# Kernel optimization log

Measured on AMD Instinct MI355X. Metric: run time of the kernel, lower is better.

Reference implementation:

```python
import jax, jax.numpy as jnp
import numpy as np

V = np.array([[1.0, 1.0, 1.0], [1.0, -1.0, 1.0], [1.0, 1.0, -1.0]], dtype=np.float32)


def _lin_combs(kernels: np.ndarray) -> np.ndarray:
    """Project (O, C, 3, 3) kernels onto inverse of the 9x9 GCK +/-1 basis.
    Returns (O, C*9) with layout c*9 + (3*i + j), matching the torch module."""
    O, C = kernels.shape[0], kernels.shape[1]
    # basis_flat[k=3i+j, p=3r+s] = V[i,r] * V[j,s]
    basis_flat = np.einsum('ir,js->ijrs', V, V).reshape(9, 9)
    basis_inv = np.linalg.inv(basis_flat)
    kflat = kernels.reshape(O, C, 9)
    comb = np.einsum('kp,ocp->ock', basis_inv, kflat)  # (O, C, 9)
    return np.ascontiguousarray(comb.reshape(O, C * 9))


def setup_inputs() -> dict:
    key = jax.random.key(0)
    k1, k2 = jax.random.split(key)
    B, C, O, H, W = 1, 64, 64, 514, 514
    x = jax.random.normal(k1, (B, C, H, W), dtype=jnp.float32)
    kernels = np.asarray(jax.random.normal(k2, (O, C, 3, 3), dtype=jnp.float32))
    linCombs = jnp.asarray(_lin_combs(kernels))  # (O, C*9)
    return {"input": x, "linCombs": linCombs}


def reference(input, linCombs):
    # GCK 3x3 conv: rowwise +/-1 stage -> colwise +/-1 stage -> linComb matmul.
    x = input
    B, C, H, W = x.shape
    O = linCombs.shape[0]
    Ho, Wo = H - 2, W - 2  # padding = 0
    Vj = jnp.asarray(V)
    # rowwise stage: convolve (cross-correlate) along rows with each +/-1 vector
    rows = jnp.stack([x[:, :, r:r + Ho, :] for r in range(3)])       # (3,B,C,Ho,W)
    rowwise = jnp.einsum('ir,rbchw->bcihw', Vj, rows)                 # (B,C,3,Ho,W)
    # colwise stage: convolve along columns with each +/-1 vector
    cols = jnp.stack([rowwise[..., s:s + Wo] for s in range(3)])      # (3,B,C,3,Ho,Wo)
    colwise = jnp.einsum('js,sbcihw->bcijhw', Vj, cols)               # (B,C,3,3,Ho,Wo)
    feats = colwise.reshape(B, C * 9, Ho * Wo)                        # k = c*9 + 3i + j
    out = jnp.einsum('ok,bkp->bop', linCombs, feats)
    return out.reshape(B, O, Ho, Wo)
```

## Files before the change

### kernel.cpp

```cpp
#include <hip/hip_runtime.h>
#include <hip/hip_bf16.h>


constexpr int kC = 64, kO = 64;
constexpr int kH = 514, kW = 514;
constexpr int kHO = 512, kWO = 512;
constexpr int kNPIX = kH * kW;

typedef __attribute__((ext_vector_type(8))) short short8;
typedef __attribute__((ext_vector_type(4))) float floatx4;

__device__ inline unsigned short f2bf(float f) {
    unsigned int u = __float_as_uint(f);
    unsigned int r = (u + 0x7fffu + ((u >> 16) & 1u)) >> 16;
    return (unsigned short)r;
}

__global__ void gck_wprep(const float* __restrict__ lin, unsigned short* __restrict__ w2) {
    int t = blockIdx.x * 256 + threadIdx.x;
    if (t >= kO * kC * 9) return;
    int tap = t % 9;
    int c   = (t / 9) % kC;
    int o   = t / (9 * kC);
    int r = tap / 3, s = tap % 3;
    const float Vm[3][3] = {{1.f, 1.f, 1.f}, {1.f, -1.f, 1.f}, {1.f, 1.f, -1.f}};
    float acc = 0.f;
#pragma unroll
    for (int i = 0; i < 3; i++)
#pragma unroll
        for (int j = 0; j < 3; j++)
            acc += lin[o * (kC * 9) + c * 9 + 3 * i + j] * Vm[i][r] * Vm[j][s];
    int kglob = tap * 64 + c;
    int ks = kglob >> 5, kg = (kglob >> 3) & 3, e = kglob & 7;
    w2[((ks * 4 + kg) * 64 + o) * 8 + e] = f2bf(acc);
}

__global__ __launch_bounds__(256, 3) void gck_conv(const float* __restrict__ x,
                                                   const unsigned short* __restrict__ w2,
                                                   float* __restrict__ out) {
    __shared__ unsigned short xs[6 * 66 * 64];

    const int bid = blockIdx.x;
    const int ct = bid & 7;
    const int rt = bid >> 3;
    const int hbase = rt * 4;
    const int wbase = ct * 64;
    const int t    = threadIdx.x;
    const int wave = t >> 6;
    const int lane = t & 63;
    const int l16  = lane & 15;
    const int kg   = lane >> 4;

    {
        const int w0 = lane;
#pragma unroll
        for (int p = 0; p < 24; ++p) {
            int idx = p * 4 + wave;
            int r   = idx >> 4;
            int cg  = idx & 15;
            int ch0 = cg * 4;
            const float* gp = x + (hbase + r) * kW + wbase + w0;
            float f0 = gp[(ch0 + 0) * kNPIX];
            float f1 = gp[(ch0 + 1) * kNPIX];
            float f2 = gp[(ch0 + 2) * kNPIX];
            float f3 = gp[(ch0 + 3) * kNPIX];
            ushort4 v;
            v.x = f2bf(f0); v.y = f2bf(f1); v.z = f2bf(f2); v.w = f2bf(f3);
            int addr = (r * 66 + w0) * 64 + ((cg >> 1) ^ (w0 & 7)) * 8 + (cg & 1) * 4;
            *reinterpret_cast<ushort4*>(&xs[addr]) = v;
        }
#pragma unroll
        for (int j = 0; j < 3; ++j) {
            int idx = j * 256 + t;
            int col = 64 + (idx & 1);
            int ch  = (idx >> 1) & 63;
            int r   = idx >> 7;
            float f = x[ch * kNPIX + (hbase + r) * kW + wbase + col];
            int addr = (r * 66 + col) * 64 + ((ch >> 3) ^ (col & 7)) * 8 + (ch & 7);
            xs[addr] = f2bf(f);
        }
    }
    __syncthreads();

    floatx4 acc[4][4];
#pragma unroll
    for (int m = 0; m < 4; m++)
#pragma unroll
        for (int n = 0; n < 4; n++) acc[m][n] = (floatx4){0.f, 0.f, 0.f, 0.f};

    const short8* w2v = reinterpret_cast<const short8*>(w2);

    short8 a_cur[4];
#pragma unroll
    for (int m = 0; m < 4; m++) a_cur[m] = w2v[(0 * 4 + kg) * 64 + m * 16 + l16];

#pragma unroll 2
    for (int ks = 0; ks < 18; ++ks) {
        int tap = ks >> 1;
        int r0  = tap / 3;
        int s   = tap - r0 * 3;

        short8 a_nxt[4];
        int ksn = (ks < 17) ? ks + 1 : ks;
#pragma unroll
        for (int m = 0; m < 4; m++) a_nxt[m] = w2v[(ksn * 4 + kg) * 64 + m * 16 + l16];

        int rr = wave + r0;
        int u  = (ks & 1) * 4 + kg;
        short8 b[4];
#pragma unroll
        for (int n = 0; n < 4; ++n) {
            int col  = n * 16 + l16 + s;
            int addr = (rr * 66 + col) * 64 + ((u ^ (col & 7)) * 8);
            b[n] = *reinterpret_cast<const short8*>(&xs[addr]);
        }

#pragma unroll
        for (int m = 0; m < 4; m++)
#pragma unroll
            for (int n = 0; n < 4; n++)
                acc[m][n] = __builtin_amdgcn_mfma_f32_16x16x32_bf16(a_cur[m], b[n], acc[m][n], 0, 0, 0);

#pragma unroll
        for (int m = 0; m < 4; m++) a_cur[m] = a_nxt[m];
    }

    const int h = hbase + wave;
#pragma unroll
    for (int m = 0; m < 4; m++) {
#pragma unroll
        for (int n = 0; n < 4; n++) {
            int wcol = wbase + n * 16 + l16;
#pragma unroll
            for (int j = 0; j < 4; j++) {
                int o = m * 16 + kg * 4 + j;
                out[(o * kHO + h) * kWO + wcol] = acc[m][n][j];
            }
        }
    }
}

extern "C" void kernel_launch(void* const* d_in, const int* in_sizes, int n_in,
                              void* d_out, int out_size, void* d_ws, size_t ws_size,
                              hipStream_t stream) {
    const float* x   = (const float*)d_in[0];
    const float* lin = (const float*)d_in[1];
    float* out = (float*)d_out;

    unsigned short* w2 = (unsigned short*)d_ws;

    gck_wprep<<<(kO * kC * 9 + 255) / 256, 256, 0, stream>>>(lin, w2);
    gck_conv<<<(kHO / 4) * 8, 256, 0, stream>>>(x, w2, out);
}
```

Before: 142.2 us.

## Shrink conv tile to two output rows and split output channels across waves

```diff
diff --git a/kernel.cpp b/kernel.cpp
--- a/kernel.cpp
+++ b/kernel.cpp
@@ -6,6 +6,7 @@
 constexpr int kH = 514, kW = 514;
 constexpr int kHO = 512, kWO = 512;
 constexpr int kNPIX = kH * kW;
+constexpr int LCOLS = 66;
 
 typedef __attribute__((ext_vector_type(8))) short short8;
 typedef __attribute__((ext_vector_type(4))) float floatx4;
@@ -35,64 +36,70 @@
     w2[((ks * 4 + kg) * 64 + o) * 8 + e] = f2bf(acc);
 }
 
-__global__ __launch_bounds__(256, 3) void gck_conv(const float* __restrict__ x,
+__global__ __launch_bounds__(256, 4) void gck_conv(const float* __restrict__ x,
                                                    const unsigned short* __restrict__ w2,
                                                    float* __restrict__ out) {
-    __shared__ unsigned short xs[6 * 66 * 64];
+    __shared__ unsigned short xs[4 * LCOLS * 64];
 
     const int bid = blockIdx.x;
     const int ct = bid & 7;
     const int rt = bid >> 3;
-    const int hbase = rt * 4;
+    const int hbase = rt * 2;
     const int wbase = ct * 64;
     const int t    = threadIdx.x;
     const int wave = t >> 6;
     const int lane = t & 63;
     const int l16  = lane & 15;
     const int kg   = lane >> 4;
+    const int hw   = wave >> 1;
+    const int o0   = (wave & 1) * 32;
 
     {
-        const int w0 = lane;
+        const int cp  = t & 31;
+        const int cg  = t >> 5;
+        const int ch0 = cg * 8;
+        const int colb = cp * 2;
 #pragma unroll
-        for (int p = 0; p < 24; ++p) {
-            int idx = p * 4 + wave;
-            int r   = idx >> 4;
-            int cg  = idx & 15;
-            int ch0 = cg * 4;
-            const float* gp = x + (hbase + r) * kW + wbase + w0;
-            float f0 = gp[(ch0 + 0) * kNPIX];
-            float f1 = gp[(ch0 + 1) * kNPIX];
-            float f2 = gp[(ch0 + 2) * kNPIX];
-            float f3 = gp[(ch0 + 3) * kNPIX];
-            ushort4 v;
-            v.x = f2bf(f0); v.y = f2bf(f1); v.z = f2bf(f2); v.w = f2bf(f3);
-            int addr = (r * 66 + w0) * 64 + ((cg >> 1) ^ (w0 & 7)) * 8 + (cg & 1) * 4;
-            *reinterpret_cast<ushort4*>(&xs[addr]) = v;
+        for (int r = 0; r < 4; ++r) {
+            const float* gp = x + (size_t)(hbase + r) * kW + wbase + colb;
+            float2 f[8];
+#pragma unroll
+            for (int c = 0; c < 8; ++c)
+                f[c] = *reinterpret_cast<const float2*>(gp + (size_t)(ch0 + c) * kNPIX);
+#pragma unroll
+            for (int j = 0; j < 2; ++j) {
+                int col = colb + j;
+                short8 u8;
+#pragma unroll
+                for (int c = 0; c < 8; ++c) u8[c] = (short)f2bf(j ? f[c].y : f[c].x);
+                int swz = (cg ^ (col & 7) ^ ((col >> 3) & 7)) & 7;
+                *reinterpret_cast<short8*>(&xs[(r * LCOLS + col) * 64 + swz * 8]) = u8;
+            }
         }
 #pragma unroll
-        for (int j = 0; j < 3; ++j) {
+        for (int j = 0; j < 2; ++j) {
             int idx = j * 256 + t;
             int col = 64 + (idx & 1);
             int ch  = (idx >> 1) & 63;
             int r   = idx >> 7;
-            float f = x[ch * kNPIX + (hbase + r) * kW + wbase + col];
-            int addr = (r * 66 + col) * 64 + ((ch >> 3) ^ (col & 7)) * 8 + (ch & 7);
-            xs[addr] = f2bf(f);
+            float f = x[(size_t)ch * kNPIX + (size_t)(hbase + r) * kW + wbase + col];
+            int swz = ((ch >> 3) ^ (col & 7) ^ ((col >> 3) & 7)) & 7;
+            xs[(r * LCOLS + col) * 64 + swz * 8 + (ch & 7)] = f2bf(f);
         }
     }
     __syncthreads();
 
-    floatx4 acc[4][4];
+    floatx4 acc[2][4];
 #pragma unroll
-    for (int m = 0; m < 4; m++)
+    for (int m = 0; m < 2; m++)
 #pragma unroll
         for (int n = 0; n < 4; n++) acc[m][n] = (floatx4){0.f, 0.f, 0.f, 0.f};
 
     const short8* w2v = reinterpret_cast<const short8*>(w2);
 
-    short8 a_cur[4];
+    short8 a_cur[2];
 #pragma unroll
-    for (int m = 0; m < 4; m++) a_cur[m] = w2v[(0 * 4 + kg) * 64 + m * 16 + l16];
+    for (int m = 0; m < 2; m++) a_cur[m] = w2v[(0 * 4 + kg) * 64 + o0 + m * 16 + l16];
 
 #pragma unroll 2
     for (int ks = 0; ks < 18; ++ks) {
@@ -100,41 +107,41 @@
         int r0  = tap / 3;
         int s   = tap - r0 * 3;
 
-        short8 a_nxt[4];
+        short8 a_nxt[2];
         int ksn = (ks < 17) ? ks + 1 : ks;
 #pragma unroll
-        for (int m = 0; m < 4; m++) a_nxt[m] = w2v[(ksn * 4 + kg) * 64 + m * 16 + l16];
+        for (int m = 0; m < 2; m++) a_nxt[m] = w2v[(ksn * 4 + kg) * 64 + o0 + m * 16 + l16];
 
-        int rr = wave + r0;
+        int rr = hw + r0;
         int u  = (ks & 1) * 4 + kg;
         short8 b[4];
 #pragma unroll
         for (int n = 0; n < 4; ++n) {
             int col  = n * 16 + l16 + s;
-            int addr = (rr * 66 + col) * 64 + ((u ^ (col & 7)) * 8);
-            b[n] = *reinterpret_cast<const short8*>(&xs[addr]);
+            int swz  = (u ^ (col & 7) ^ ((col >> 3) & 7)) & 7;
+            b[n] = *reinterpret_cast<const short8*>(&xs[(rr * LCOLS + col) * 64 + swz * 8]);
         }
 
 #pragma unroll
-        for (int m = 0; m < 4; m++)
+        for (int m = 0; m < 2; m++)
 #pragma unroll
             for (int n = 0; n < 4; n++)
                 acc[m][n] = __builtin_amdgcn_mfma_f32_16x16x32_bf16(a_cur[m], b[n], acc[m][n], 0, 0, 0);
 
 #pragma unroll
-        for (int m = 0; m < 4; m++) a_cur[m] = a_nxt[m];
+        for (int m = 0; m < 2; m++) a_cur[m] = a_nxt[m];
     }
 
-    const int h = hbase + wave;
+    const int h = hbase + hw;
 #pragma unroll
-    for (int m = 0; m < 4; m++) {
+    for (int m = 0; m < 2; m++) {
 #pragma unroll
         for (int n = 0; n < 4; n++) {
             int wcol = wbase + n * 16 + l16;
 #pragma unroll
             for (int j = 0; j < 4; j++) {
-                int o = m * 16 + kg * 4 + j;
-                out[(o * kHO + h) * kWO + wcol] = acc[m][n][j];
+                int o = o0 + m * 16 + kg * 4 + j;
+                out[((size_t)o * kHO + h) * kWO + wcol] = acc[m][n][j];
             }
         }
     }
@@ -150,5 +157,5 @@
     unsigned short* w2 = (unsigned short*)d_ws;
 
     gck_wprep<<<(kO * kC * 9 + 255) / 256, 256, 0, stream>>>(lin, w2);
-    gck_conv<<<(kHO / 4) * 8, 256, 0, stream>>>(x, w2, out);
+    gck_conv<<<(kHO / 2) * 8, 256, 0, stream>>>(x, w2, out);
 }
```

Result: no change. 142.2 us (+0.0%).
